# Performance work log

Measured on AMD Instinct MI355X. Metric: run time of the kernel, lower is better.

The kernel has to match this reference:

```python
import jax, jax.numpy as jnp
import numpy as np
from jax import lax

B, C, H, W = 16, 128, 64, 64
S = 16  # d_state


def setup_inputs() -> dict:
    key = jax.random.key(0)
    ks = jax.random.split(key, 12)
    d = {
        'x': jax.random.normal(ks[0], (B, C, H, W), jnp.float32),
        'conv_w': jax.random.normal(ks[1], (C, C, 3, 3), jnp.float32) * (1.0 / np.sqrt(C * 9)),
        'conv_b': jax.random.normal(ks[2], (C,), jnp.float32) * 0.01,
        'dt_w': jax.random.normal(ks[3], (C, C), jnp.float32) * (1.0 / np.sqrt(C)),
        'dt_b': jax.random.normal(ks[4], (C,), jnp.float32) * 0.01,
        'A': jax.random.normal(ks[5], (C, S), jnp.float32),
        'D': jax.random.normal(ks[6], (C,), jnp.float32),
        'g1_w': jax.random.normal(ks[7], (C, C), jnp.float32) * (1.0 / np.sqrt(C)),
        'g1_b': jax.random.normal(ks[8], (C,), jnp.float32) * 0.01,
        'g2_w': jax.random.normal(ks[9], (C, C), jnp.float32) * (1.0 / np.sqrt(C)),
        'g2_b': jax.random.normal(ks[10], (C,), jnp.float32) * 0.01,
    }
    return d


def _forward(x, conv_w, conv_b, dt_w, dt_b, A, D, g1_w, g1_b, g2_w, g2_b):
    identity = x
    # 3x3 conv, padding=1 (SAME)
    x = lax.conv_general_dilated(x, conv_w, (1, 1), 'SAME',
                                 dimension_numbers=('NCHW', 'OIHW', 'NCHW'))
    x = x + conv_b[None, :, None, None]
    # spectral gate: global avg pool -> 1x1 conv -> relu -> 1x1 conv -> sigmoid
    pooled = jnp.mean(x, axis=(2, 3))                       # [B, C]
    g = jax.nn.relu(jnp.einsum('bc,oc->bo', pooled, g1_w) + g1_b)
    g = jax.nn.sigmoid(jnp.einsum('bc,oc->bo', g, g2_w) + g2_b)
    x = x * g[:, :, None, None]
    # ssm scan over H*W tokens
    x_seq = x.transpose(0, 2, 3, 1).reshape(x.shape[0], H * W, C)  # [B, L, C]
    dt = jax.nn.sigmoid(jnp.einsum('blc,oc->blo', x_seq, dt_w) + dt_b)
    An = -jnp.exp(A)   # [C, S]
    Dp = jnp.exp(D)    # [C]

    def step(h, inp):
        xt, dtt = inp  # each [B, C]
        h = h * jnp.exp(An[None] * dtt[:, :, None]) + xt[:, :, None]  # [B, C, S]
        y = jnp.sum(h * An[None], axis=-1) + Dp * xt                   # [B, C]
        return h, y

    h0 = jnp.zeros((x.shape[0], C, S), x.dtype)
    xs = (x_seq.transpose(1, 0, 2), dt.transpose(1, 0, 2))  # [L, B, C]
    _, ys = lax.scan(step, h0, xs)                           # ys: [L, B, C]
    y = ys.transpose(1, 0, 2).reshape(x.shape[0], H, W, C).transpose(0, 3, 1, 2)
    return y + identity


def reference(x, conv_w, conv_b, dt_w, dt_b, A, D, g1_w, g1_b, g2_w, g2_b):
    return _forward(x, conv_w, conv_b, dt_w, dt_b, A, D, g1_w, g1_b, g2_w, g2_b)
```

## Files before the change

kernel.cpp:

```cpp
#include <hip/hip_runtime.h>
#include <hip/hip_bf16.h>
#include <stdint.h>

#define BB 16
#define CC 128
#define HH 64
#define WW 64
#define LL 4096
#define SS 16
#define NCH 64
#define CT 64

typedef __attribute__((ext_vector_type(4))) float f32x4;
typedef __attribute__((ext_vector_type(8))) short short8;
typedef __attribute__((ext_vector_type(4))) unsigned int u32x4;

#define AS1 __attribute__((address_space(1)))
#define AS3 __attribute__((address_space(3)))

__device__ __forceinline__ float bf2f(unsigned short u) {
    union { unsigned int i; float f; } v;
    v.i = ((unsigned int)u) << 16;
    return v.f;
}
__device__ __forceinline__ unsigned short f2bf(float f) {
    union { float f; unsigned int i; } v;
    v.f = f;
    unsigned int x = v.i;
    return (unsigned short)((x + 0x7fffu + ((x >> 16) & 1u)) >> 16);
}
__device__ __forceinline__ float fexp2(float x) { return __builtin_amdgcn_exp2f(x); }

__global__ __launch_bounds__(256) void k0(const float* __restrict__ x, unsigned short* __restrict__ xT,
                                          const float* __restrict__ conv_w, const float* __restrict__ dt_w,
                                          const float* __restrict__ A, const float* __restrict__ Dv,
                                          const float* __restrict__ g1w, const float* __restrict__ g2w,
                                          short* __restrict__ wf, short* __restrict__ wdtf,
                                          float* __restrict__ An, float* __restrict__ An2, float* __restrict__ Dp,
                                          float* __restrict__ pooled, float* __restrict__ g1wT, float* __restrict__ g2wT) {
    __shared__ float lt[64][65];
    int bid = blockIdx.x;
    int tid = threadIdx.x;
    if (bid < 2048) {
        int b = bid >> 7, rem = bid & 127;
        int tt = rem >> 1, ct = rem & 1;
        int t0 = tt * 64, c0 = ct * 64;
        int colr = tid & 63, rowb = tid >> 6;
#pragma unroll
        for (int r = 0; r < 16; ++r) {
            int row = rowb + r * 4;
            lt[row][colr] = x[(size_t)(b * CC + c0 + row) * LL + t0 + colr];
        }
        __syncthreads();
#pragma unroll
        for (int r = 0; r < 16; ++r) {
            int trow = rowb + r * 4;
            xT[((size_t)b * LL + t0 + trow) * CC + c0 + colr] = f2bf(lt[colr][trow]);
        }
        return;
    }
    int idx = (bid - 2048) * 256 + tid;
    if (idx < 18432) {
        int lane = idx & 63, fr = idx >> 6;
        int nfg = fr & 7, ks = (fr >> 3) & 3, tp = fr >> 5;
        int dy = tp / 3, dx = tp % 3;
        int cout = nfg * 16 + (lane & 15);
        int cin0 = ks * 32 + (lane >> 4) * 8;
        short8 v;
#pragma unroll
        for (int j = 0; j < 8; ++j)
            v[j] = (short)f2bf(conv_w[((cout * CC + cin0 + j) * 3 + dy) * 3 + dx]);
        *(short8*)(wf + (size_t)idx * 8) = v;
    } else if (idx < 20480) {
        int i2 = idx - 18432;
        int lane = i2 & 63, fr = i2 >> 6;
        int nfg = fr & 7, ks = fr >> 3;
        int o = nfg * 16 + (lane & 15);
        int c0 = ks * 32 + (lane >> 4) * 8;
        short8 v;
#pragma unroll
        for (int j = 0; j < 8; ++j) v[j] = (short)f2bf(dt_w[o * CC + c0 + j]);
        *(short8*)(wdtf + (size_t)i2 * 8) = v;
    } else if (idx < 22528) {
        int i3 = idx - 20480;
        float a = -expf(A[i3]);
        An[i3] = a;
        An2[i3] = a * 1.4426950408889634f;
    } else if (idx < 22656) {
        int c = idx - 22528;
        Dp[c] = expf(Dv[c]);
    } else if (idx < 24704) {
        pooled[idx - 22656] = 0.f;
    } else if (idx < 41088) {
        int i = idx - 24704;
        int c = i >> 7, o = i & 127;
        g1wT[i] = g1w[o * 128 + c];
    } else if (idx < 57472) {
        int i = idx - 41088;
        int c = i >> 7, o = i & 127;
        g2wT[i] = g2w[o * 128 + c];
    }
}

__global__ __launch_bounds__(256) void k1(const unsigned short* __restrict__ xT,
                                          const short* __restrict__ wf,
                                          const float* __restrict__ conv_b,
                                          unsigned short* __restrict__ convT,
                                          float* __restrict__ pooled) {
    __shared__ __align__(16) unsigned short slab[3 * 66 * 128];
    int bid = blockIdx.x;
    int b = bid >> 6, h = bid & 63;
    int tid = threadIdx.x;
    int wave = tid >> 6, lane = tid & 63;

    if (tid < 96) {
        int dy = tid >> 5, r = (tid >> 4) & 1, j = tid & 15;
        u32x4 z = {0, 0, 0, 0};
        *(u32x4*)((char*)slab + dy * 16896 + (r ? 16640 : 0) + j * 16) = z;
    }
#pragma unroll
    for (int dy = 0; dy < 3; ++dy) {
        int hs = h + dy - 1;
        char* slabdy = (char*)slab + dy * 16896;
        if (hs >= 0 && hs < HH) {
            const char* src = (const char*)xT + (size_t)(b * LL + hs * 64) * 256;
#pragma unroll
            for (int i = 0; i < 4; ++i) {
                unsigned int Xbase = 256u + (unsigned)i * 4096u + (unsigned)wave * 1024u;
                unsigned int X = Xbase + (unsigned)lane * 16u;
                unsigned int tok = X >> 8;
                unsigned int srcoff = ((X & ~255u) - 256u) | ((X & 255u) ^ ((tok & 7u) << 4));
                __builtin_amdgcn_global_load_lds((const AS1 unsigned int*)(src + srcoff),
                                                 (AS3 unsigned int*)(slabdy + Xbase), 16, 0, 0);
            }
        } else {
            u32x4 z = {0, 0, 0, 0};
#pragma unroll
            for (int i = 0; i < 4; ++i)
                *(u32x4*)(slabdy + 256 + tid * 64 + i * 16) = z;
        }
    }
    __syncthreads();

    int lm = lane & 15, lg = lane >> 4;
    f32x4 acc[4][2];
#pragma unroll
    for (int m = 0; m < 4; ++m)
#pragma unroll
        for (int n = 0; n < 2; ++n) acc[m][n] = (f32x4){0.f, 0.f, 0.f, 0.f};

#pragma unroll
    for (int tp = 0; tp < 9; ++tp) {
        int dy = tp / 3, dx = tp % 3;
        const char* slabdy = (const char*)slab + dy * 16896;
#pragma unroll
        for (int ks = 0; ks < 4; ++ks) {
            short8 bf0 = *(const short8*)(wf + ((size_t)(((tp * 4 + ks) * 8) + wave * 2 + 0) * 64 + lane) * 8);
            short8 bf1 = *(const short8*)(wf + ((size_t)(((tp * 4 + ks) * 8) + wave * 2 + 1) * 64 + lane) * 8);
#pragma unroll
            for (int mf = 0; mf < 4; ++mf) {
                int tok = mf * 16 + lm + dx;
                unsigned int off = (unsigned)((tok * 256 + ks * 64 + lg * 16) ^ ((tok & 7) << 4));
                short8 af = *(const short8*)(slabdy + off);
                acc[mf][0] = __builtin_amdgcn_mfma_f32_16x16x32_bf16(af, bf0, acc[mf][0], 0, 0, 0);
                acc[mf][1] = __builtin_amdgcn_mfma_f32_16x16x32_bf16(af, bf1, acc[mf][1], 0, 0, 0);
            }
        }
    }

    int n0w = wave * 32;
    size_t tokbase = (size_t)(b * LL + h * 64);
    float psum[2] = {0.f, 0.f};
#pragma unroll
    for (int nf = 0; nf < 2; ++nf) {
        int n = n0w + nf * 16 + lm;
        float bias = conv_b[n];
#pragma unroll
        for (int mf = 0; mf < 4; ++mf)
#pragma unroll
            for (int r = 0; r < 4; ++r) {
                int w = mf * 16 + lg * 4 + r;
                float v = acc[mf][nf][r] + bias;
                convT[(tokbase + w) * CC + n] = f2bf(v);
                psum[nf] += v;
            }
    }
#pragma unroll
    for (int nf = 0; nf < 2; ++nf) {
        float s = psum[nf];
        s += __shfl_xor(s, 16);
        s += __shfl_xor(s, 32);
        if (lane < 16) atomicAdd(&pooled[b * CC + n0w + nf * 16 + lane], s);
    }
}

__global__ __launch_bounds__(256) void k3(const unsigned short* __restrict__ convT,
                                          const short* __restrict__ wdtf,
                                          const float* __restrict__ pooled,
                                          const float* __restrict__ g1wT, const float* __restrict__ g1b,
                                          const float* __restrict__ g2wT, const float* __restrict__ g2b,
                                          float* __restrict__ gate,
                                          const float* __restrict__ dt_b,
                                          const float* __restrict__ An2,
                                          unsigned short* __restrict__ dtT,
                                          float* __restrict__ hend, float* __restrict__ decay) {
    __shared__ __align__(16) unsigned short albuf[128 * 128];
    __shared__ __align__(16) unsigned short dtl[128 * 136];
    __shared__ float gl[128];
    float* meanr = (float*)dtl;
    float* garr  = ((float*)dtl) + 128;
    int bid = blockIdx.x;
    int b = bid >> 5, tile = bid & 31, t0 = tile * 128;
    int tid = threadIdx.x;
    int wave = tid >> 6, lane = tid & 63;

    if (tid < 128) meanr[tid] = pooled[b * CC + tid] * (1.f / 4096.f);
    __syncthreads();
    if (tid < 128) {
        float acc = g1b[tid];
        for (int c = 0; c < 128; ++c) acc += meanr[c] * g1wT[c * 128 + tid];
        garr[tid] = fmaxf(acc, 0.f);
    }
    __syncthreads();
    if (tid < 128) {
        float acc2 = g2b[tid];
        for (int c = 0; c < 128; ++c) acc2 += garr[c] * g2wT[c * 128 + tid];
        float gv = __builtin_amdgcn_rcpf(1.f + fexp2(-1.4426950408889634f * acc2));
        gl[tid] = gv;
        if (tile == 0) gate[b * CC + tid] = gv;
    }
    __syncthreads();

    const char* srcb = (const char*)convT + (size_t)(b * LL + t0) * 256;
#pragma unroll
    for (int i = 0; i < 8; ++i) {
        unsigned int byteoff = (unsigned)((i * 256 + tid) * 16);
        unsigned int tok = byteoff >> 8;
        unsigned int inner = byteoff & 255u;
        int c8 = (int)(inner >> 1);
        short8 v = *(const short8*)(srcb + (size_t)tok * 256 + inner);
#pragma unroll
        for (int j = 0; j < 8; ++j) {
            float f = bf2f((unsigned short)v[j]) * gl[c8 + j];
            v[j] = (short)f2bf(f);
        }
        *(short8*)((char*)albuf + (byteoff ^ ((tok & 7u) << 4))) = v;
    }
    __syncthreads();

    int lm = lane & 15, lg = lane >> 4;
    f32x4 acc[8][2];
#pragma unroll
    for (int m = 0; m < 8; ++m)
#pragma unroll
        for (int n = 0; n < 2; ++n) acc[m][n] = (f32x4){0.f, 0.f, 0.f, 0.f};
#pragma unroll
    for (int ks = 0; ks < 4; ++ks) {
        short8 bf0 = *(const short8*)(wdtf + ((size_t)((ks * 8) + wave * 2 + 0) * 64 + lane) * 8);
        short8 bf1 = *(const short8*)(wdtf + ((size_t)((ks * 8) + wave * 2 + 1) * 64 + lane) * 8);
#pragma unroll
        for (int mf = 0; mf < 8; ++mf) {
            int tok = mf * 16 + lm;
            unsigned int off = (unsigned)((tok * 256 + ks * 64 + lg * 16) ^ ((tok & 7) << 4));
            short8 af = *(const short8*)((const char*)albuf + off);
            acc[mf][0] = __builtin_amdgcn_mfma_f32_16x16x32_bf16(af, bf0, acc[mf][0], 0, 0, 0);
            acc[mf][1] = __builtin_amdgcn_mfma_f32_16x16x32_bf16(af, bf1, acc[mf][1], 0, 0, 0);
        }
    }
    __syncthreads();
#pragma unroll
    for (int nf = 0; nf < 2; ++nf) {
        int o = wave * 32 + nf * 16 + lm;
        float zb = dt_b[o];
#pragma unroll
        for (int mf = 0; mf < 8; ++mf)
#pragma unroll
            for (int r = 0; r < 4; ++r) {
                int tok = mf * 16 + lg * 4 + r;
                float z = acc[mf][nf][r] + zb;
                float d = __builtin_amdgcn_rcpf(1.f + fexp2(-1.4426950408889634f * z));
                unsigned short ub = f2bf(d);
                dtT[(size_t)(b * LL + t0 + tok) * CC + o] = ub;
                dtl[tok * 136 + o] = ub;
            }
    }
    __syncthreads();

    int half = tid >> 7, c = tid & 127;
    int ch = tile * 2 + half;
    float a2[SS], h[SS];
#pragma unroll
    for (int s = 0; s < SS; ++s) {
        a2[s] = An2[c * SS + s];
        h[s] = 0.f;
    }
    float sdt = 0.f;
#pragma unroll 4
    for (int t = 0; t < CT; ++t) {
        int tokb = half * 64 + t;
        unsigned int xoff = ((unsigned)(tokb * 256 + c * 2)) ^ (((unsigned)tokb & 7u) << 4);
        float x = bf2f(*(const unsigned short*)((const char*)albuf + xoff));
        float d = bf2f(dtl[tokb * 136 + c]);
        sdt += d;
#pragma unroll
        for (int s = 0; s < SS; ++s) h[s] = h[s] * fexp2(a2[s] * d) + x;
    }
    size_t base = ((size_t)(b * NCH + ch) * CC + c) * SS;
#pragma unroll
    for (int q = 0; q < 4; ++q) {
        f32x4 hv, dv;
#pragma unroll
        for (int j = 0; j < 4; ++j) {
            hv[j] = h[q * 4 + j];
            dv[j] = fexp2(a2[q * 4 + j] * sdt);
        }
        *(f32x4*)(hend + base + q * 4) = hv;
        *(f32x4*)(decay + base + q * 4) = dv;
    }
}

__global__ __launch_bounds__(256) void k5(const float* __restrict__ hend, const float* __restrict__ decay,
                                          float* __restrict__ H0) {
    int idx = blockIdx.x * 256 + threadIdx.x;
    int b = idx >> 11, rem = idx & 2047;
    float Hv = 0.f;
    for (int k = 0; k < NCH; ++k) {
        size_t base = (size_t)(b * NCH + k) * 2048 + rem;
        H0[base] = Hv;
        Hv = hend[base] + Hv * decay[base];
    }
}

__global__ __launch_bounds__(256, 4) void k6(const unsigned short* __restrict__ convT,
                                             const unsigned short* __restrict__ dtT,
                                             const float* __restrict__ gate,
                                             const float* __restrict__ Antab,
                                             const float* __restrict__ An2tab,
                                             const float* __restrict__ Dp,
                                             const float* __restrict__ H0,
                                             const float* __restrict__ xin,
                                             float* __restrict__ out) {
    __shared__ unsigned short ylds[128][66];
    int bid = blockIdx.x;
    int b = bid >> 6, ch = bid & 63;
    int tid = threadIdx.x;
    int wave = tid >> 6, lane = tid & 63;
    int t0 = ch * CT;
    int c = wave * 32 + (lane & 31);
    int shalf = lane >> 5;
    int s0 = shalf * 8;

    float a2[8], an[8], h[8];
#pragma unroll
    for (int q = 0; q < 2; ++q) {
        f32x4 av = *(const f32x4*)(An2tab + c * SS + s0 + q * 4);
        f32x4 nv = *(const f32x4*)(Antab + c * SS + s0 + q * 4);
#pragma unroll
        for (int j = 0; j < 4; ++j) { a2[q * 4 + j] = av[j]; an[q * 4 + j] = nv[j]; }
    }
    size_t hbase = ((size_t)(b * NCH + ch) * CC + c) * SS + s0;
#pragma unroll
    for (int q = 0; q < 2; ++q) {
        f32x4 hv = *(const f32x4*)(H0 + hbase + q * 4);
#pragma unroll
        for (int j = 0; j < 4; ++j) h[q * 4 + j] = hv[j];
    }
    float g = gate[b * CC + c];
    float dpc = (shalf == 0) ? Dp[c] : 0.f;
    const unsigned short* xp = convT + (size_t)(b * LL + t0) * CC + c;
    const unsigned short* dp = dtT + (size_t)(b * LL + t0) * CC + c;

#pragma unroll 4
    for (int t = 0; t < CT; ++t) {
        float x = bf2f(xp[t * CC]) * g;
        float d = bf2f(dp[t * CC]);
        float y0 = dpc * x, y1 = 0.f;
#pragma unroll
        for (int s = 0; s < 8; ++s) {
            h[s] = h[s] * fexp2(a2[s] * d) + x;
            if (s & 1) y1 += h[s] * an[s]; else y0 += h[s] * an[s];
        }
        float yp = y0 + y1;
        float yo = yp + __shfl_xor(yp, 32);
        if (shalf == 0) ylds[c][t] = f2bf(yo);
    }
    __syncthreads();

    int tt = tid & 63, wq = tid >> 6;
    size_t outbase = (size_t)b * CC * LL + t0 + tt;
#pragma unroll 4
    for (int rr = 0; rr < 32; ++rr) {
        int row = rr * 4 + wq;
        size_t gi = outbase + (size_t)row * LL;
        out[gi] = bf2f(ylds[row][tt]) + xin[gi];
    }
}

extern "C" void kernel_launch(void* const* d_in, const int* in_sizes, int n_in,
                              void* d_out, int out_size, void* d_ws, size_t ws_size,
                              hipStream_t stream) {
    const float* x      = (const float*)d_in[0];
    const float* conv_w = (const float*)d_in[1];
    const float* conv_b = (const float*)d_in[2];
    const float* dt_w   = (const float*)d_in[3];
    const float* dt_b   = (const float*)d_in[4];
    const float* A      = (const float*)d_in[5];
    const float* D      = (const float*)d_in[6];
    const float* g1w    = (const float*)d_in[7];
    const float* g1b    = (const float*)d_in[8];
    const float* g2w    = (const float*)d_in[9];
    const float* g2b    = (const float*)d_in[10];

    char* ws = (char*)d_ws;
    unsigned short* xT    = (unsigned short*)(ws + 0);
    float* hend           = (float*)(ws + 0);
    float* decay          = (float*)(ws + 8388608);
    unsigned short* convT = (unsigned short*)(ws + 16777216);
    unsigned short* dtT   = (unsigned short*)(ws + 33554432);
    float* H0             = (float*)(ws + 50331648);
    float* g1wT           = (float*)(ws + 50331648);
    float* g2wT           = (float*)(ws + 50397184);
    short* wf             = (short*)(ws + 58720256);
    short* wdtf           = (short*)(ws + 59015168);
    float* pooled         = (float*)(ws + 59047936);
    float* gate           = (float*)(ws + 59056128);
    float* Antab          = (float*)(ws + 59064320);
    float* An2tab         = (float*)(ws + 59072512);
    float* Dp             = (float*)(ws + 59080704);
    float* outp           = (float*)d_out;

    hipLaunchKernelGGL(k0, dim3(2273), dim3(256), 0, stream, x, xT, conv_w, dt_w, A, D, g1w, g2w,
                       wf, wdtf, Antab, An2tab, Dp, pooled, g1wT, g2wT);
    hipLaunchKernelGGL(k1, dim3(1024), dim3(256), 0, stream, xT, wf, conv_b, convT, pooled);
    hipLaunchKernelGGL(k3, dim3(512), dim3(256), 0, stream, convT, wdtf, pooled, g1wT, g1b, g2wT, g2b,
                       gate, dt_b, An2tab, dtT, hend, decay);
    hipLaunchKernelGGL(k5, dim3(128), dim3(256), 0, stream, hend, decay, H0);
    hipLaunchKernelGGL(k6, dim3(1024), dim3(256), 0, stream, convT, dtT, gate, Antab, An2tab, Dp, H0, x, outp);
}
```

Measured before the change: 125.5 us.

## Pack gated x and dt into channel-major words for final scan pass

```diff
diff --git a/kernel.cpp b/kernel.cpp
--- a/kernel.cpp
+++ b/kernel.cpp
@@ -11,6 +11,7 @@
 #define NCH 64
 #define CT 64
 
+typedef __attribute__((ext_vector_type(2))) float f32x2;
 typedef __attribute__((ext_vector_type(4))) float f32x4;
 typedef __attribute__((ext_vector_type(8))) short short8;
 typedef __attribute__((ext_vector_type(4))) unsigned int u32x4;
@@ -21,6 +22,11 @@
 __device__ __forceinline__ float bf2f(unsigned short u) {
     union { unsigned int i; float f; } v;
     v.i = ((unsigned int)u) << 16;
+    return v.f;
+}
+__device__ __forceinline__ float asf(unsigned int u) {
+    union { unsigned int i; float f; } v;
+    v.i = u;
     return v.f;
 }
 __device__ __forceinline__ unsigned short f2bf(float f) {
@@ -203,7 +209,9 @@
                                           const float* __restrict__ dt_b,
                                           const float* __restrict__ An2,
                                           unsigned short* __restrict__ dtT,
-                                          float* __restrict__ hend, float* __restrict__ decay) {
+                                          unsigned int* __restrict__ xdt,
+                                          float* __restrict__ hend, float* __restrict__ decay,
+                                          int packed) {
     __shared__ __align__(16) unsigned short albuf[128 * 128];
     __shared__ __align__(16) unsigned short dtl[128 * 136];
     __shared__ float gl[128];
@@ -280,7 +288,7 @@
                 float z = acc[mf][nf][r] + zb;
                 float d = __builtin_amdgcn_rcpf(1.f + fexp2(-1.4426950408889634f * z));
                 unsigned short ub = f2bf(d);
-                dtT[(size_t)(b * LL + t0 + tok) * CC + o] = ub;
+                if (!packed) dtT[(size_t)(b * LL + t0 + tok) * CC + o] = ub;
                 dtl[tok * 136 + o] = ub;
             }
     }
@@ -295,15 +303,24 @@
         h[s] = 0.f;
     }
     float sdt = 0.f;
-#pragma unroll 4
-    for (int t = 0; t < CT; ++t) {
-        int tokb = half * 64 + t;
-        unsigned int xoff = ((unsigned)(tokb * 256 + c * 2)) ^ (((unsigned)tokb & 7u) << 4);
-        float x = bf2f(*(const unsigned short*)((const char*)albuf + xoff));
-        float d = bf2f(dtl[tokb * 136 + c]);
-        sdt += d;
-#pragma unroll
-        for (int s = 0; s < SS; ++s) h[s] = h[s] * fexp2(a2[s] * d) + x;
+    unsigned int* xdrow = xdt + ((size_t)b * CC + c) * LL + t0 + half * 64;
+    for (int t4 = 0; t4 < 16; ++t4) {
+        u32x4 pk;
+#pragma unroll
+        for (int j = 0; j < 4; ++j) {
+            int t = t4 * 4 + j;
+            int tokb = half * 64 + t;
+            unsigned int xoff = ((unsigned)(tokb * 256 + c * 2)) ^ (((unsigned)tokb & 7u) << 4);
+            unsigned short xu = *(const unsigned short*)((const char*)albuf + xoff);
+            unsigned short du = dtl[tokb * 136 + c];
+            float x = bf2f(xu);
+            float d = bf2f(du);
+            sdt += d;
+#pragma unroll
+            for (int s = 0; s < SS; ++s) h[s] = h[s] * fexp2(a2[s] * d) + x;
+            pk[j] = (((unsigned int)du) << 16) | (unsigned int)xu;
+        }
+        if (packed) *(u32x4*)(xdrow + t4 * 4) = pk;
     }
     size_t base = ((size_t)(b * NCH + ch) * CC + c) * SS;
 #pragma unroll
@@ -331,15 +348,89 @@
     }
 }
 
-__global__ __launch_bounds__(256, 4) void k6(const unsigned short* __restrict__ convT,
-                                             const unsigned short* __restrict__ dtT,
-                                             const float* __restrict__ gate,
-                                             const float* __restrict__ Antab,
-                                             const float* __restrict__ An2tab,
-                                             const float* __restrict__ Dp,
-                                             const float* __restrict__ H0,
-                                             const float* __restrict__ xin,
-                                             float* __restrict__ out) {
+__global__ __launch_bounds__(256, 4) void k6p(const unsigned int* __restrict__ xdt,
+                                              const float* __restrict__ Antab,
+                                              const float* __restrict__ An2tab,
+                                              const float* __restrict__ Dp,
+                                              const float* __restrict__ H0,
+                                              const float* __restrict__ xin,
+                                              float* __restrict__ out) {
+    __shared__ unsigned short ylds[128][66];
+    int bid = blockIdx.x;
+    int b = bid >> 6, ch = bid & 63;
+    int tid = threadIdx.x;
+    int wave = tid >> 6, lane = tid & 63;
+    int t0 = ch * CT;
+    int c = wave * 32 + (lane & 31);
+    int shalf = lane >> 5;
+    int s0 = shalf * 8;
+
+    f32x2 a22[4], anv[4], h2[4];
+#pragma unroll
+    for (int q = 0; q < 2; ++q) {
+        f32x4 av = *(const f32x4*)(An2tab + c * SS + s0 + q * 4);
+        f32x4 nv = *(const f32x4*)(Antab + c * SS + s0 + q * 4);
+        a22[q * 2 + 0] = (f32x2){av[0], av[1]};
+        a22[q * 2 + 1] = (f32x2){av[2], av[3]};
+        anv[q * 2 + 0] = (f32x2){nv[0], nv[1]};
+        anv[q * 2 + 1] = (f32x2){nv[2], nv[3]};
+    }
+    size_t hbase = ((size_t)(b * NCH + ch) * CC + c) * SS + s0;
+#pragma unroll
+    for (int q = 0; q < 2; ++q) {
+        f32x4 hv = *(const f32x4*)(H0 + hbase + q * 4);
+        h2[q * 2 + 0] = (f32x2){hv[0], hv[1]};
+        h2[q * 2 + 1] = (f32x2){hv[2], hv[3]};
+    }
+    float dpc = (shalf == 0) ? Dp[c] : 0.f;
+    const u32x4* xdp = (const u32x4*)(xdt + ((size_t)b * CC + c) * LL + t0);
+
+#pragma unroll 4
+    for (int t4 = 0; t4 < 16; ++t4) {
+        u32x4 w4 = xdp[t4];
+#pragma unroll
+        for (int j = 0; j < 4; ++j) {
+            unsigned int w = w4[j];
+            float x = asf(w << 16);
+            float d = asf(w & 0xffff0000u);
+            f32x2 x2 = {x, x};
+            f32x2 d2 = {d, d};
+            f32x2 y2 = {0.f, 0.f};
+#pragma unroll
+            for (int q = 0; q < 4; ++q) {
+                f32x2 tq = a22[q] * d2;
+                f32x2 e2;
+                e2.x = fexp2(tq.x);
+                e2.y = fexp2(tq.y);
+                h2[q] = h2[q] * e2 + x2;
+                y2 += h2[q] * anv[q];
+            }
+            float yp = y2.x + y2.y + dpc * x;
+            float yo = yp + __shfl_xor(yp, 32);
+            if (shalf == 0) ylds[c][t4 * 4 + j] = f2bf(yo);
+        }
+    }
+    __syncthreads();
+
+    int tt = tid & 63, wq = tid >> 6;
+    size_t outbase = (size_t)b * CC * LL + t0 + tt;
+#pragma unroll 4
+    for (int rr = 0; rr < 32; ++rr) {
+        int row = rr * 4 + wq;
+        size_t gi = outbase + (size_t)row * LL;
+        out[gi] = bf2f(ylds[row][tt]) + xin[gi];
+    }
+}
+
+__global__ __launch_bounds__(256, 4) void k6f(const unsigned short* __restrict__ convT,
+                                              const unsigned short* __restrict__ dtT,
+                                              const float* __restrict__ gate,
+                                              const float* __restrict__ Antab,
+                                              const float* __restrict__ An2tab,
+                                              const float* __restrict__ Dp,
+                                              const float* __restrict__ H0,
+                                              const float* __restrict__ xin,
+                                              float* __restrict__ out) {
     __shared__ unsigned short ylds[128][66];
     int bid = blockIdx.x;
     int b = bid >> 6, ch = bid & 63;
@@ -410,30 +501,64 @@
     const float* g1b    = (const float*)d_in[8];
     const float* g2w    = (const float*)d_in[9];
     const float* g2b    = (const float*)d_in[10];
-
+    float* outp         = (float*)d_out;
     char* ws = (char*)d_ws;
-    unsigned short* xT    = (unsigned short*)(ws + 0);
-    float* hend           = (float*)(ws + 0);
-    float* decay          = (float*)(ws + 8388608);
-    unsigned short* convT = (unsigned short*)(ws + 16777216);
-    unsigned short* dtT   = (unsigned short*)(ws + 33554432);
-    float* H0             = (float*)(ws + 50331648);
-    float* g1wT           = (float*)(ws + 50331648);
-    float* g2wT           = (float*)(ws + 50397184);
-    short* wf             = (short*)(ws + 58720256);
-    short* wdtf           = (short*)(ws + 59015168);
-    float* pooled         = (float*)(ws + 59047936);
-    float* gate           = (float*)(ws + 59056128);
-    float* Antab          = (float*)(ws + 59064320);
-    float* An2tab         = (float*)(ws + 59072512);
-    float* Dp             = (float*)(ws + 59080704);
-    float* outp           = (float*)d_out;
+
+    const bool P = (ws_size >= 67600896ull);
+
+    unsigned short* xT;
+    float *hend, *decay, *H0, *g1wT, *g2wT, *pooled, *gate, *Antab, *An2tab, *Dp;
+    unsigned short *convT, *dtT;
+    unsigned int* xdt;
+    short *wf, *wdtf;
+
+    if (P) {
+        xT     = (unsigned short*)(ws + 0);
+        hend   = (float*)(ws + 0);
+        decay  = (float*)(ws + 8388608);
+        convT  = (unsigned short*)(ws + 16777216);
+        H0     = (float*)(ws + 16777216);
+        xdt    = (unsigned int*)(ws + 33554432);
+        dtT    = (unsigned short*)(ws + 33554432);
+        wf     = (short*)(ws + 67108864);
+        wdtf   = (short*)(ws + 67403776);
+        pooled = (float*)(ws + 67436544);
+        gate   = (float*)(ws + 67444736);
+        Antab  = (float*)(ws + 67452928);
+        An2tab = (float*)(ws + 67461120);
+        Dp     = (float*)(ws + 67469312);
+        g1wT   = (float*)(ws + 67469824);
+        g2wT   = (float*)(ws + 67535360);
+    } else {
+        xT     = (unsigned short*)(ws + 0);
+        hend   = (float*)(ws + 0);
+        decay  = (float*)(ws + 8388608);
+        convT  = (unsigned short*)(ws + 16777216);
+        dtT    = (unsigned short*)(ws + 33554432);
+        xdt    = (unsigned int*)(ws + 33554432);
+        H0     = (float*)(ws + 50331648);
+        g1wT   = (float*)(ws + 50331648);
+        g2wT   = (float*)(ws + 50397184);
+        wf     = (short*)(ws + 58720256);
+        wdtf   = (short*)(ws + 59015168);
+        pooled = (float*)(ws + 59047936);
+        gate   = (float*)(ws + 59056128);
+        Antab  = (float*)(ws + 59064320);
+        An2tab = (float*)(ws + 59072512);
+        Dp     = (float*)(ws + 59080704);
+    }
 
     hipLaunchKernelGGL(k0, dim3(2273), dim3(256), 0, stream, x, xT, conv_w, dt_w, A, D, g1w, g2w,
                        wf, wdtf, Antab, An2tab, Dp, pooled, g1wT, g2wT);
     hipLaunchKernelGGL(k1, dim3(1024), dim3(256), 0, stream, xT, wf, conv_b, convT, pooled);
     hipLaunchKernelGGL(k3, dim3(512), dim3(256), 0, stream, convT, wdtf, pooled, g1wT, g1b, g2wT, g2b,
-                       gate, dt_b, An2tab, dtT, hend, decay);
+                       gate, dt_b, An2tab, dtT, xdt, hend, decay, (int)P);
     hipLaunchKernelGGL(k5, dim3(128), dim3(256), 0, stream, hend, decay, H0);
-    hipLaunchKernelGGL(k6, dim3(1024), dim3(256), 0, stream, convT, dtT, gate, Antab, An2tab, Dp, H0, x, outp);
-}
+    if (P) {
+        hipLaunchKernelGGL(k6p, dim3(1024), dim3(256), 0, stream, (const unsigned int*)xdt,
+                           Antab, An2tab, Dp, H0, x, outp);
+    } else {
+        hipLaunchKernelGGL(k6f, dim3(1024), dim3(256), 0, stream, convT, dtT, gate,
+                           Antab, An2tab, Dp, H0, x, outp);
+    }
+}
```

New measurement: 120.9 us, median of 2. -3.6%, faster.
